# Kernel tuning notes

Measured on AMD Instinct MI355X. Metric: run time of the kernel, lower is better.

## Reference

```python
import jax, jax.numpy as jnp
import numpy as np

DIM = 1024
HEADS = 16
HEAD_DIM = DIM // HEADS
MAX_SEQ = 4096
BATCH = 16
POSITION = MAX_SEQ - 1


def setup_inputs() -> dict:
    key = jax.random.key(0)
    ks = jax.random.split(key, 8)
    s = 0.02  # weight init scale, typical for transformer linears
    return {
        "token": jax.random.normal(ks[0], (BATCH, 1, DIM), dtype=jnp.float32),
        "k_cache": jax.random.normal(ks[1], (BATCH, MAX_SEQ, HEADS, HEAD_DIM), dtype=jnp.float32),
        "v_cache": jax.random.normal(ks[2], (BATCH, MAX_SEQ, HEADS, HEAD_DIM), dtype=jnp.float32),
        "Wq": jax.random.normal(ks[3], (DIM, DIM), dtype=jnp.float32) * s,
        "Wk": jax.random.normal(ks[4], (DIM, DIM), dtype=jnp.float32) * s,
        "Wv": jax.random.normal(ks[5], (DIM, DIM), dtype=jnp.float32) * s,
        "Wo": jax.random.normal(ks[6], (DIM, DIM), dtype=jnp.float32) * s,
        "position": POSITION,
    }


def reference(token, k_cache, v_cache, Wq, Wk, Wv, Wo, position):
    # Decode step: single-query attention against KV cache (FlexDecodingModule.decode).
    B = token.shape[0]
    # QKV projections (torch Linear: x @ W.T), bias=False
    q = (token @ Wq.T).reshape(B, 1, HEADS, HEAD_DIM)
    k = (token @ Wk.T).reshape(B, 1, HEADS, HEAD_DIM)
    v = (token @ Wv.T).reshape(B, 1, HEADS, HEAD_DIM)
    # Inline KV-cache append at `position` (static python int)
    kc = k_cache.at[:, position].set(k[:, 0])
    vc = v_cache.at[:, position].set(v[:, 0])
    past_k = kc[:, : position + 1]  # [B, L, H, D]
    past_v = vc[:, : position + 1]
    # Causal score_mod with offset=position, q_idx=0 => all kv_idx<=position visible (no mask)
    scale = 1.0 / np.sqrt(HEAD_DIM).astype(np.float32)
    scores = jnp.einsum("bqhd,bkhd->bhqk", q, past_k) * scale  # [B, H, 1, L]
    attn = jax.nn.softmax(scores, axis=-1)
    out = jnp.einsum("bhqk,bkhd->bqhd", attn, past_v)  # [B, 1, H, D]
    out = out.reshape(B, 1, DIM)
    return out @ Wo.T
```

## Files before the change

kernel.cpp:

```cpp
#include <hip/hip_runtime.h>
#include <hip/hip_bf16.h>
#include <math.h>

#define DIM 1024
#define HEADS 16
#define HEAD_DIM 64
#define MAXSEQ 4096
#define BATCH 16
#define CHUNK 64
#define NCHUNK (MAXSEQ / CHUNK)
#define TILE 8

__global__ __launch_bounds__(256) void qkv_proj(
    const float* __restrict__ token,
    const float* __restrict__ Wq, const float* __restrict__ Wk,
    const float* __restrict__ Wv,
    float* __restrict__ out ) {
  __shared__ float tok[BATCH * DIM];
  for (int idx = threadIdx.x; idx < BATCH * DIM; idx += 256)
    tok[idx] = token[idx];
  __syncthreads();

  const float* W = (blockIdx.y == 0) ? Wq : ((blockIdx.y == 1) ? Wk : Wv);
  float* o = out + (size_t)blockIdx.y * BATCH * DIM;

  const int wave = threadIdx.x >> 6;
  const int lane = threadIdx.x & 63;
  const int i0 = blockIdx.x * 16 + wave * 4;

  float acc[4][16];
#pragma unroll
  for (int ii = 0; ii < 4; ++ii)
#pragma unroll
    for (int b = 0; b < 16; ++b) acc[ii][b] = 0.f;

  for (int t = 0; t < 16; ++t) {
    const int j = t * 64 + lane;
    float tk[16];
#pragma unroll
    for (int b = 0; b < 16; ++b) tk[b] = tok[b * DIM + j];
#pragma unroll
    for (int ii = 0; ii < 4; ++ii) {
      const float w = W[(size_t)(i0 + ii) * DIM + j];
#pragma unroll
      for (int b = 0; b < 16; ++b) acc[ii][b] = fmaf(w, tk[b], acc[ii][b]);
    }
  }

#pragma unroll
  for (int ii = 0; ii < 4; ++ii)
#pragma unroll
    for (int b = 0; b < 16; ++b) {
      float v = acc[ii][b];
#pragma unroll
      for (int m = 32; m >= 1; m >>= 1) v += __shfl_xor(v, m);
      if (lane == 0) o[(size_t)b * DIM + i0 + ii] = v;
    }
}

__global__ __launch_bounds__(256) void attn_partial(
    const float* __restrict__ kc, const float* __restrict__ vc,
    const float* __restrict__ qkv, const int* __restrict__ pos_p,
    float* __restrict__ part) {
  const int c = blockIdx.x, b = blockIdx.y;
  const int t = threadIdx.x;
  const int h = t >> 4, lq = t & 15;
  const int pos = pos_p[0];
  const int nk = pos + 1;
  const int s0 = c * CHUNK;

  const float* qp   = qkv + (size_t)b * DIM;
  const float* knew = qkv + (size_t)BATCH * DIM + (size_t)b * DIM;
  const float* vnew = qkv + 2 * (size_t)BATCH * DIM + (size_t)b * DIM;
  const float* kbase = kc + (size_t)b * MAXSEQ * DIM;
  const float* vbase = vc + (size_t)b * MAXSEQ * DIM;

  const float scale = 0.125f;
  float4 q4 = *(const float4*)(qp + 4 * t);
  q4.x *= scale; q4.y *= scale; q4.z *= scale; q4.w *= scale;

  float m = -INFINITY, l = 0.f;
  float4 a4 = make_float4(0.f, 0.f, 0.f, 0.f);

  for (int i0 = 0; i0 < CHUNK; i0 += TILE) {
    float4 k4[TILE], v4[TILE];
#pragma unroll
    for (int j = 0; j < TILE; ++j) {
      const int s = s0 + i0 + j;
      const float* krow = (s == pos) ? knew : (kbase + (size_t)s * DIM);
      const float* vrow = (s == pos) ? vnew : (vbase + (size_t)s * DIM);
      k4[j] = *(const float4*)(krow + 4 * t);
      v4[j] = *(const float4*)(vrow + 4 * t);
    }

    float sc[TILE];
#pragma unroll
    for (int j = 0; j < TILE; ++j)
      sc[j] = q4.x * k4[j].x + q4.y * k4[j].y + q4.z * k4[j].z +
              q4.w * k4[j].w;

#pragma unroll
    for (int j = 0; j < TILE; ++j) {
      sc[j] += __shfl_xor(sc[j], 1);
      sc[j] += __shfl_xor(sc[j], 2);
      sc[j] += __shfl_xor(sc[j], 4);
      sc[j] += __shfl_xor(sc[j], 8);
    }
#pragma unroll
    for (int j = 0; j < TILE; ++j)
      if (s0 + i0 + j >= nk) sc[j] = -INFINITY;

    float tm = sc[0];
#pragma unroll
    for (int j = 1; j < TILE; ++j) tm = fmaxf(tm, sc[j]);
    const float m_new = fmaxf(m, tm);
    const float corr = (m_new == -INFINITY) ? 1.f : __expf(m - m_new);
    l *= corr;
    a4.x *= corr; a4.y *= corr; a4.z *= corr; a4.w *= corr;
    m = m_new;

#pragma unroll
    for (int j = 0; j < TILE; ++j) {
      const float p = (sc[j] == -INFINITY) ? 0.f : __expf(sc[j] - m);
      l += p;
      a4.x = fmaf(p, v4[j].x, a4.x);
      a4.y = fmaf(p, v4[j].y, a4.y);
      a4.z = fmaf(p, v4[j].z, a4.z);
      a4.w = fmaf(p, v4[j].w, a4.w);
    }
  }

  const size_t base = (((size_t)(b * HEADS + h)) * NCHUNK + c) * 66;
  part[base + 2 + lq * 4 + 0] = a4.x;
  part[base + 2 + lq * 4 + 1] = a4.y;
  part[base + 2 + lq * 4 + 2] = a4.z;
  part[base + 2 + lq * 4 + 3] = a4.w;
  if (lq == 0) { part[base] = m; part[base + 1] = l; }
}

__global__ __launch_bounds__(64) void attn_combine(
    const float* __restrict__ part, float* __restrict__ attn) {
  const int bh = blockIdx.x;
  const int b = bh >> 4, h = bh & 15;
  const int d = threadIdx.x;
  const float* p0 = part + (size_t)bh * NCHUNK * 66;
  float M = -INFINITY;
#pragma unroll
  for (int c = 0; c < NCHUNK; ++c) M = fmaxf(M, p0[c * 66]);
  float L = 0.f, o = 0.f;
#pragma unroll 8
  for (int c = 0; c < NCHUNK; ++c) {
    const float mc = p0[c * 66];
    if (mc > -INFINITY) {
      const float w = __expf(mc - M);
      L += p0[c * 66 + 1] * w;
      o = fmaf(p0[c * 66 + 2 + d], w, o);
    }
  }
  attn[(size_t)b * DIM + h * HEAD_DIM + d] = o / L;
}

__global__ __launch_bounds__(256) void o_proj(
    const float* __restrict__ attn, const float* __restrict__ Wo,
    float* __restrict__ out) {
  __shared__ float tok[BATCH * DIM];
  for (int idx = threadIdx.x; idx < BATCH * DIM; idx += 256)
    tok[idx] = attn[idx];
  __syncthreads();

  const int wave = threadIdx.x >> 6;
  const int lane = threadIdx.x & 63;
  const int i0 = blockIdx.x * 16 + wave * 4;

  float acc[4][16];
#pragma unroll
  for (int ii = 0; ii < 4; ++ii)
#pragma unroll
    for (int b = 0; b < 16; ++b) acc[ii][b] = 0.f;

  for (int t = 0; t < 16; ++t) {
    const int j = t * 64 + lane;
    float tk[16];
#pragma unroll
    for (int b = 0; b < 16; ++b) tk[b] = tok[b * DIM + j];
#pragma unroll
    for (int ii = 0; ii < 4; ++ii) {
      const float w = Wo[(size_t)(i0 + ii) * DIM + j];
#pragma unroll
      for (int b = 0; b < 16; ++b) acc[ii][b] = fmaf(w, tk[b], acc[ii][b]);
    }
  }

#pragma unroll
  for (int ii = 0; ii < 4; ++ii)
#pragma unroll
    for (int b = 0; b < 16; ++b) {
      float v = acc[ii][b];
#pragma unroll
      for (int m = 32; m >= 1; m >>= 1) v += __shfl_xor(v, m);
      if (lane == 0) out[(size_t)b * DIM + i0 + ii] = v;
    }
}

extern "C" void kernel_launch(void* const* d_in, const int* in_sizes, int n_in,
                              void* d_out, int out_size, void* d_ws, size_t ws_size,
                              hipStream_t stream) {
  const float* token = (const float*)d_in[0];
  const float* kc = (const float*)d_in[1];
  const float* vc = (const float*)d_in[2];
  const float* Wq = (const float*)d_in[3];
  const float* Wk = (const float*)d_in[4];
  const float* Wv = (const float*)d_in[5];
  const float* Wo = (const float*)d_in[6];
  const int* pos = (const int*)d_in[7];
  float* out = (float*)d_out;
  float* ws = (float*)d_ws;

  float* qkv = ws;
  float* part = ws + 3 * BATCH * DIM;
  float* attn = part + (size_t)BATCH * HEADS * NCHUNK * 66;

  hipLaunchKernelGGL(qkv_proj, dim3(64, 3), dim3(256), 0, stream,
                     token, Wq, Wk, Wv, qkv);
  hipLaunchKernelGGL(attn_partial, dim3(NCHUNK, BATCH), dim3(256), 0,
                     stream, kc, vc, qkv, pos, part);
  hipLaunchKernelGGL(attn_combine, dim3(BATCH * HEADS), dim3(64), 0, stream,
                     part, attn);
  hipLaunchKernelGGL(o_proj, dim3(64), dim3(256), 0, stream, attn, Wo, out);
  (void)in_sizes; (void)n_in; (void)out_size; (void)ws_size;
}
```

Measured before the change: 167.2 us.

## Double-buffer KV tiles via async global-to-LDS loads in attention partial kernel

```diff
diff --git a/kernel.cpp b/kernel.cpp
--- a/kernel.cpp
+++ b/kernel.cpp
@@ -9,7 +9,14 @@
 #define BATCH 16
 #define CHUNK 64
 #define NCHUNK (MAXSEQ / CHUNK)
-#define TILE 8
+#define TROWS 4
+#define NTILE (CHUNK / TROWS)
+
+__device__ __forceinline__ void gload_lds16(const float* g, float* l) {
+  __builtin_amdgcn_global_load_lds(
+      (const __attribute__((address_space(1))) void*)g,
+      (__attribute__((address_space(3))) void*)l, 16, 0, 0);
+}
 
 __global__ __launch_bounds__(256) void qkv_proj(
     const float* __restrict__ token,
@@ -58,16 +65,19 @@
     }
 }
 
-__global__ __launch_bounds__(256) void attn_partial(
+__global__ __launch_bounds__(256, 2) void attn_partial(
     const float* __restrict__ kc, const float* __restrict__ vc,
     const float* __restrict__ qkv, const int* __restrict__ pos_p,
     float* __restrict__ part) {
   const int c = blockIdx.x, b = blockIdx.y;
   const int t = threadIdx.x;
+  const int w = t >> 6, lane = t & 63;
   const int h = t >> 4, lq = t & 15;
   const int pos = pos_p[0];
   const int nk = pos + 1;
   const int s0 = c * CHUNK;
+
+  __shared__ __align__(16) float smem[4][2][2][TROWS][256];
 
   const float* qp   = qkv + (size_t)b * DIM;
   const float* knew = qkv + (size_t)BATCH * DIM + (size_t)b * DIM;
@@ -78,55 +88,75 @@
   const float scale = 0.125f;
   float4 q4 = *(const float4*)(qp + 4 * t);
   q4.x *= scale; q4.y *= scale; q4.z *= scale; q4.w *= scale;
-
-  float m = -INFINITY, l = 0.f;
+  __builtin_amdgcn_sched_barrier(0);
+
+  auto stage = [&](int j, int p) {
+#pragma unroll
+    for (int r = 0; r < TROWS; ++r) {
+      const int s = s0 + j * TROWS + r;
+      const float* kg = (s == pos) ? knew : (kbase + (size_t)s * DIM);
+      const float* vg = (s == pos) ? vnew : (vbase + (size_t)s * DIM);
+      gload_lds16(kg + (w << 8) + (lane << 2), &smem[w][p][0][r][0]);
+      gload_lds16(vg + (w << 8) + (lane << 2), &smem[w][p][1][r][0]);
+    }
+  };
+
+  stage(0, 0);
+  stage(1, 1);
+
+  float m = -INFINITY, lsum = 0.f;
   float4 a4 = make_float4(0.f, 0.f, 0.f, 0.f);
 
-  for (int i0 = 0; i0 < CHUNK; i0 += TILE) {
-    float4 k4[TILE], v4[TILE];
-#pragma unroll
-    for (int j = 0; j < TILE; ++j) {
-      const int s = s0 + i0 + j;
-      const float* krow = (s == pos) ? knew : (kbase + (size_t)s * DIM);
-      const float* vrow = (s == pos) ? vnew : (vbase + (size_t)s * DIM);
-      k4[j] = *(const float4*)(krow + 4 * t);
-      v4[j] = *(const float4*)(vrow + 4 * t);
-    }
-
-    float sc[TILE];
-#pragma unroll
-    for (int j = 0; j < TILE; ++j)
-      sc[j] = q4.x * k4[j].x + q4.y * k4[j].y + q4.z * k4[j].z +
-              q4.w * k4[j].w;
-
-#pragma unroll
-    for (int j = 0; j < TILE; ++j) {
-      sc[j] += __shfl_xor(sc[j], 1);
-      sc[j] += __shfl_xor(sc[j], 2);
-      sc[j] += __shfl_xor(sc[j], 4);
-      sc[j] += __shfl_xor(sc[j], 8);
-    }
-#pragma unroll
-    for (int j = 0; j < TILE; ++j)
-      if (s0 + i0 + j >= nk) sc[j] = -INFINITY;
-
-    float tm = sc[0];
-#pragma unroll
-    for (int j = 1; j < TILE; ++j) tm = fmaxf(tm, sc[j]);
+  for (int j = 0; j < NTILE; ++j) {
+    const int p = j & 1;
+    asm volatile("s_waitcnt vmcnt(8)" ::: "memory");
+    __builtin_amdgcn_sched_barrier(0);
+
+    float4 k4[TROWS], v4[TROWS];
+#pragma unroll
+    for (int r = 0; r < TROWS; ++r) {
+      k4[r] = *(const float4*)&smem[w][p][0][r][lane << 2];
+      v4[r] = *(const float4*)&smem[w][p][1][r][lane << 2];
+    }
+    asm volatile("s_waitcnt lgkmcnt(0)" ::: "memory");
+    __builtin_amdgcn_sched_barrier(0);
+
+    const int jn = (j + 2 < NTILE) ? (j + 2) : (NTILE - 1);
+    stage(jn, p);
+    __builtin_amdgcn_sched_barrier(0);
+
+    float sc[TROWS];
+#pragma unroll
+    for (int r = 0; r < TROWS; ++r)
+      sc[r] = q4.x * k4[r].x + q4.y * k4[r].y + q4.z * k4[r].z +
+              q4.w * k4[r].w;
+#pragma unroll
+    for (int r = 0; r < TROWS; ++r) {
+      sc[r] += __shfl_xor(sc[r], 1);
+      sc[r] += __shfl_xor(sc[r], 2);
+      sc[r] += __shfl_xor(sc[r], 4);
+      sc[r] += __shfl_xor(sc[r], 8);
+    }
+    const int srow = s0 + j * TROWS;
+#pragma unroll
+    for (int r = 0; r < TROWS; ++r)
+      if (srow + r >= nk) sc[r] = -INFINITY;
+
+    float tm = fmaxf(fmaxf(sc[0], sc[1]), fmaxf(sc[2], sc[3]));
     const float m_new = fmaxf(m, tm);
     const float corr = (m_new == -INFINITY) ? 1.f : __expf(m - m_new);
-    l *= corr;
+    lsum *= corr;
     a4.x *= corr; a4.y *= corr; a4.z *= corr; a4.w *= corr;
     m = m_new;
 
 #pragma unroll
-    for (int j = 0; j < TILE; ++j) {
-      const float p = (sc[j] == -INFINITY) ? 0.f : __expf(sc[j] - m);
-      l += p;
-      a4.x = fmaf(p, v4[j].x, a4.x);
-      a4.y = fmaf(p, v4[j].y, a4.y);
-      a4.z = fmaf(p, v4[j].z, a4.z);
-      a4.w = fmaf(p, v4[j].w, a4.w);
+    for (int r = 0; r < TROWS; ++r) {
+      const float pp = (sc[r] == -INFINITY) ? 0.f : __expf(sc[r] - m);
+      lsum += pp;
+      a4.x = fmaf(pp, v4[r].x, a4.x);
+      a4.y = fmaf(pp, v4[r].y, a4.y);
+      a4.z = fmaf(pp, v4[r].z, a4.z);
+      a4.w = fmaf(pp, v4[r].w, a4.w);
     }
   }
 
@@ -135,7 +165,7 @@
   part[base + 2 + lq * 4 + 1] = a4.y;
   part[base + 2 + lq * 4 + 2] = a4.z;
   part[base + 2 + lq * 4 + 3] = a4.w;
-  if (lq == 0) { part[base] = m; part[base + 1] = l; }
+  if (lq == 0) { part[base] = m; part[base + 1] = lsum; }
 }
 
 __global__ __launch_bounds__(64) void attn_combine(
```

Result: slower. 177.7 us (+6.3%).

## Split attention into finer sequence blocks and fold new KV token into combine

Applied to the files above, without the earlier changes.

```diff
diff --git a/kernel.cpp b/kernel.cpp
--- a/kernel.cpp
+++ b/kernel.cpp
@@ -7,9 +7,9 @@
 #define HEAD_DIM 64
 #define MAXSEQ 4096
 #define BATCH 16
-#define CHUNK 64
-#define NCHUNK (MAXSEQ / CHUNK)
-#define TILE 8
+#define SEQ_PER_BLK 16
+#define NBLK (MAXSEQ / SEQ_PER_BLK)
+#define TILE 4
 
 __global__ __launch_bounds__(256) void qkv_proj(
     const float* __restrict__ token,
@@ -58,20 +58,17 @@
     }
 }
 
-__global__ __launch_bounds__(256) void attn_partial(
+__global__ __launch_bounds__(256, 8) void attn_partial(
     const float* __restrict__ kc, const float* __restrict__ vc,
     const float* __restrict__ qkv, const int* __restrict__ pos_p,
     float* __restrict__ part) {
-  const int c = blockIdx.x, b = blockIdx.y;
+  const int blk = blockIdx.x, b = blockIdx.y;
   const int t = threadIdx.x;
   const int h = t >> 4, lq = t & 15;
   const int pos = pos_p[0];
-  const int nk = pos + 1;
-  const int s0 = c * CHUNK;
-
-  const float* qp   = qkv + (size_t)b * DIM;
-  const float* knew = qkv + (size_t)BATCH * DIM + (size_t)b * DIM;
-  const float* vnew = qkv + 2 * (size_t)BATCH * DIM + (size_t)b * DIM;
+  const int s0 = blk * SEQ_PER_BLK;
+
+  const float* qp    = qkv + (size_t)b * DIM;
   const float* kbase = kc + (size_t)b * MAXSEQ * DIM;
   const float* vbase = vc + (size_t)b * MAXSEQ * DIM;
 
@@ -79,18 +76,17 @@
   float4 q4 = *(const float4*)(qp + 4 * t);
   q4.x *= scale; q4.y *= scale; q4.z *= scale; q4.w *= scale;
 
-  float m = -INFINITY, l = 0.f;
+  float m = -INFINITY, lsum = 0.f;
   float4 a4 = make_float4(0.f, 0.f, 0.f, 0.f);
 
-  for (int i0 = 0; i0 < CHUNK; i0 += TILE) {
+#pragma unroll
+  for (int tile = 0; tile < SEQ_PER_BLK / TILE; ++tile) {
     float4 k4[TILE], v4[TILE];
 #pragma unroll
     for (int j = 0; j < TILE; ++j) {
-      const int s = s0 + i0 + j;
-      const float* krow = (s == pos) ? knew : (kbase + (size_t)s * DIM);
-      const float* vrow = (s == pos) ? vnew : (vbase + (size_t)s * DIM);
-      k4[j] = *(const float4*)(krow + 4 * t);
-      v4[j] = *(const float4*)(vrow + 4 * t);
+      const int s = s0 + tile * TILE + j;
+      k4[j] = *(const float4*)(kbase + (size_t)s * DIM + 4 * t);
+      v4[j] = *(const float4*)(vbase + (size_t)s * DIM + 4 * t);
     }
 
     float sc[TILE];
@@ -98,7 +94,6 @@
     for (int j = 0; j < TILE; ++j)
       sc[j] = q4.x * k4[j].x + q4.y * k4[j].y + q4.z * k4[j].z +
               q4.w * k4[j].w;
-
 #pragma unroll
     for (int j = 0; j < TILE; ++j) {
       sc[j] += __shfl_xor(sc[j], 1);
@@ -108,21 +103,19 @@
     }
 #pragma unroll
     for (int j = 0; j < TILE; ++j)
-      if (s0 + i0 + j >= nk) sc[j] = -INFINITY;
-
-    float tm = sc[0];
-#pragma unroll
-    for (int j = 1; j < TILE; ++j) tm = fmaxf(tm, sc[j]);
+      if (s0 + tile * TILE + j >= pos) sc[j] = -INFINITY;
+
+    float tm = fmaxf(fmaxf(sc[0], sc[1]), fmaxf(sc[2], sc[3]));
     const float m_new = fmaxf(m, tm);
     const float corr = (m_new == -INFINITY) ? 1.f : __expf(m - m_new);
-    l *= corr;
+    lsum *= corr;
     a4.x *= corr; a4.y *= corr; a4.z *= corr; a4.w *= corr;
     m = m_new;
 
 #pragma unroll
     for (int j = 0; j < TILE; ++j) {
       const float p = (sc[j] == -INFINITY) ? 0.f : __expf(sc[j] - m);
-      l += p;
+      lsum += p;
       a4.x = fmaf(p, v4[j].x, a4.x);
       a4.y = fmaf(p, v4[j].y, a4.y);
       a4.z = fmaf(p, v4[j].z, a4.z);
@@ -130,26 +123,44 @@
     }
   }
 
-  const size_t base = (((size_t)(b * HEADS + h)) * NCHUNK + c) * 66;
+  const size_t base = (((size_t)(b * HEADS + h)) * NBLK + blk) * 66;
   part[base + 2 + lq * 4 + 0] = a4.x;
   part[base + 2 + lq * 4 + 1] = a4.y;
   part[base + 2 + lq * 4 + 2] = a4.z;
   part[base + 2 + lq * 4 + 3] = a4.w;
-  if (lq == 0) { part[base] = m; part[base + 1] = l; }
+  if (lq == 0) { part[base] = m; part[base + 1] = lsum; }
 }
 
 __global__ __launch_bounds__(64) void attn_combine(
-    const float* __restrict__ part, float* __restrict__ attn) {
+    const float* __restrict__ part, const float* __restrict__ qkv,
+    const int* __restrict__ pos_p, float* __restrict__ attn) {
   const int bh = blockIdx.x;
   const int b = bh >> 4, h = bh & 15;
   const int d = threadIdx.x;
-  const float* p0 = part + (size_t)bh * NCHUNK * 66;
-  float M = -INFINITY;
-#pragma unroll
-  for (int c = 0; c < NCHUNK; ++c) M = fmaxf(M, p0[c * 66]);
-  float L = 0.f, o = 0.f;
+
+  const float qd = qkv[(size_t)b * DIM + h * HEAD_DIM + d];
+  const float kd = qkv[(size_t)BATCH * DIM + (size_t)b * DIM + h * HEAD_DIM + d];
+  const float vd = qkv[2 * (size_t)BATCH * DIM + (size_t)b * DIM + h * HEAD_DIM + d];
+
+  float sn = qd * kd;
+  sn += __shfl_xor(sn, 1);
+  sn += __shfl_xor(sn, 2);
+  sn += __shfl_xor(sn, 4);
+  sn += __shfl_xor(sn, 8);
+  sn += __shfl_xor(sn, 16);
+  sn += __shfl_xor(sn, 32);
+  sn *= 0.125f;
+
+  const float* p0 = part + (size_t)bh * NBLK * 66;
+  float M = sn;
 #pragma unroll 8
-  for (int c = 0; c < NCHUNK; ++c) {
+  for (int c = 0; c < NBLK; ++c) M = fmaxf(M, p0[c * 66]);
+
+  const float wn = __expf(sn - M);
+  float L = wn;
+  float o = wn * vd;
+#pragma unroll 8
+  for (int c = 0; c < NBLK; ++c) {
     const float mc = p0[c * 66];
     if (mc > -INFINITY) {
       const float w = __expf(mc - M);
@@ -218,14 +229,14 @@
 
   float* qkv = ws;
   float* part = ws + 3 * BATCH * DIM;
-  float* attn = part + (size_t)BATCH * HEADS * NCHUNK * 66;
+  float* attn = part + (size_t)BATCH * HEADS * NBLK * 66;
 
   hipLaunchKernelGGL(qkv_proj, dim3(64, 3), dim3(256), 0, stream,
                      token, Wq, Wk, Wv, qkv);
-  hipLaunchKernelGGL(attn_partial, dim3(NCHUNK, BATCH), dim3(256), 0,
+  hipLaunchKernelGGL(attn_partial, dim3(NBLK, BATCH), dim3(256), 0,
                      stream, kc, vc, qkv, pos, part);
   hipLaunchKernelGGL(attn_combine, dim3(BATCH * HEADS), dim3(64), 0, stream,
-                     part, attn);
+                     part, qkv, pos, attn);
   hipLaunchKernelGGL(o_proj, dim3(64), dim3(256), 0, stream, attn, Wo, out);
   (void)in_sizes; (void)n_in; (void)out_size; (void)ws_size;
 }
```

After: 316.7 us. +89.5%, slower.
